# Optimization experiments

Hardware: AMD Instinct MI355X
Metric: run time of the kernel (lower is better)

## Reference

```python
import jax, jax.numpy as jnp
import numpy as np

N_NODES = 100000
N_EDGES = 3200000
D_IN = 64
D_HID = 64


def _sage_conv(x, src, dst, Wl, bl, Wr, n_nodes):
    # PyG SAGEConv (aggr='mean', root_weight=True):
    #   out = lin_l(mean_{j in N(i)} x_j) + lin_r(x_i)
    msg = x[src]                                              # [E, d] gather
    agg = jax.ops.segment_sum(msg, dst, num_segments=n_nodes) # [N, d] scatter-sum
    cnt = jax.ops.segment_sum(jnp.ones((src.shape[0],), x.dtype), dst,
                              num_segments=n_nodes)           # [N]
    agg = agg / jnp.maximum(cnt, 1.0)[:, None]                # mean (empty -> 0)
    return agg @ Wl.T + bl + x @ Wr.T


def setup_inputs() -> dict:
    key = jax.random.key(0)
    ks = jax.random.split(key, 12)
    x = jax.random.normal(ks[0], (N_NODES, D_IN), dtype=jnp.float32)
    edge_index = jax.random.randint(ks[1], (2, N_EDGES), 0, N_NODES, dtype=jnp.int64)
    s = 1.0 / np.sqrt(D_IN)
    h = 1.0 / np.sqrt(D_HID)
    params = {
        'Wl1': jax.random.uniform(ks[2], (D_HID, D_IN), jnp.float32, -s, s),
        'bl1': jnp.zeros((D_HID,), jnp.float32),
        'Wr1': jax.random.uniform(ks[3], (D_HID, D_IN), jnp.float32, -s, s),
        'Wl2': jax.random.uniform(ks[4], (D_HID, D_HID), jnp.float32, -h, h),
        'bl2': jnp.zeros((D_HID,), jnp.float32),
        'Wr2': jax.random.uniform(ks[5], (D_HID, D_HID), jnp.float32, -h, h),
        'Wl3': jax.random.uniform(ks[6], (D_HID, D_HID), jnp.float32, -h, h),
        'bl3': jnp.zeros((D_HID,), jnp.float32),
        'Wr3': jax.random.uniform(ks[7], (D_HID, D_HID), jnp.float32, -h, h),
        'Wlin': jax.random.uniform(ks[8], (1, D_HID), jnp.float32, -h, h),
        'blin': jnp.zeros((1,), jnp.float32),
    }
    return {'x': x, 'edge_index': edge_index, **params}


def reference(x, edge_index, Wl1, bl1, Wr1, Wl2, bl2, Wr2, Wl3, bl3, Wr3, Wlin, blin):
    src, dst = edge_index[0], edge_index[1]
    n = x.shape[0]
    h = _sage_conv(x, src, dst, Wl1, bl1, Wr1, n)
    h = _sage_conv(h, src, dst, Wl2, bl2, Wr2, n)
    h = _sage_conv(h, src, dst, Wl3, bl3, Wr3, n)
    # global_mean_pool with batch=None -> single graph mean over all nodes
    g = jnp.mean(h, axis=0, keepdims=True)   # [1, D_HID]
    return g @ Wlin.T + blin                 # [1, 1]
```

## Files before the change

kernel.cpp:

```cpp
#include <hip/hip_runtime.h>
#include <stdint.h>

#define D 64
#define PNBLK 512
#define NBMAX 400
#define CAPS 16
#define CAPD 32
#define XPB 512
#define XPST 272

__device__ __forceinline__ uint32_t rup8(uint32_t v) { return (v + 7u) & ~7u; }

__global__ void zero_kernel(float* __restrict__ p, int n) {
    int i = blockIdx.x * blockDim.x + threadIdx.x;
    if (i < n) p[i] = 0.0f;
}

__global__ void cnt_kernel(const int* __restrict__ dst, float* __restrict__ cnt, int ne) {
    int i = blockIdx.x * blockDim.x + threadIdx.x;
    if (i < ne) atomicAdd(&cnt[dst[i]], 1.0f);
}
__global__ void scatter_kernel(const int* __restrict__ src, const int* __restrict__ dst,
                               const float* __restrict__ r, float* __restrict__ an, int ne) {
    int i = blockIdx.x * blockDim.x + threadIdx.x;
    if (i < ne) atomicAdd(&an[src[i]], r[dst[i]]);
}
__global__ void r0_kernel(const float* __restrict__ cnt, float* __restrict__ r, int nn) {
    int i = blockIdx.x * blockDim.x + threadIdx.x;
    if (i < nn) r[i] = (1.0f / (float)nn) / fmaxf(cnt[i], 1.0f);
}
__global__ void rdiv_kernel(const float* __restrict__ a, const float* __restrict__ cnt,
                            float* __restrict__ r, int nn) {
    int i = blockIdx.x * blockDim.x + threadIdx.x;
    if (i < nn) r[i] = a[i] / fmaxf(cnt[i], 1.0f);
}

__global__ __launch_bounds__(256) void xpass_kernel(
        const float* __restrict__ x,
        const float* __restrict__ a1, const float* __restrict__ a2,
        const float* __restrict__ a3, float* __restrict__ Xpart, int nn) {
    const int tid = threadIdx.x;
    const int cg = tid & 15;
    const int rs = tid >> 4;
    float4 c0 = {0,0,0,0}, c1 = {0,0,0,0}, c2 = {0,0,0,0}, c3 = {0,0,0,0};
    float ss1 = 0.f, ss2 = 0.f;
    for (int i = blockIdx.x * 16 + rs; i < nn; i += gridDim.x * 16) {
        float4 xv = *(const float4*)(x + (size_t)i * D + cg * 4);
        float w1 = a1[i], w2 = a2[i], w3 = a3[i];
        c0.x += xv.x; c0.y += xv.y; c0.z += xv.z; c0.w += xv.w;
        c1.x = fmaf(w1, xv.x, c1.x); c1.y = fmaf(w1, xv.y, c1.y);
        c1.z = fmaf(w1, xv.z, c1.z); c1.w = fmaf(w1, xv.w, c1.w);
        c2.x = fmaf(w2, xv.x, c2.x); c2.y = fmaf(w2, xv.y, c2.y);
        c2.z = fmaf(w2, xv.z, c2.z); c2.w = fmaf(w2, xv.w, c2.w);
        c3.x = fmaf(w3, xv.x, c3.x); c3.y = fmaf(w3, xv.y, c3.y);
        c3.z = fmaf(w3, xv.z, c3.z); c3.w = fmaf(w3, xv.w, c3.w);
        if (cg == 0) { ss1 += w1; ss2 += w2; }
    }
    __shared__ float4 sm[4][16][16];
    __shared__ float sms1[16], sms2[16];
    sm[0][rs][cg] = c0; sm[1][rs][cg] = c1; sm[2][rs][cg] = c2; sm[3][rs][cg] = c3;
    if (cg == 0) { sms1[rs] = ss1; sms2[rs] = ss2; }
    __syncthreads();
    for (int s = 8; s; s >>= 1) {
        if (rs < s) {
            #pragma unroll
            for (int k = 0; k < 4; k++) {
                float4 a = sm[k][rs][cg], b = sm[k][rs + s][cg];
                a.x += b.x; a.y += b.y; a.z += b.z; a.w += b.w;
                sm[k][rs][cg] = a;
            }
            if (cg == 0) { sms1[rs] += sms1[rs + s]; sms2[rs] += sms2[rs + s]; }
        }
        __syncthreads();
    }
    float* outp = Xpart + (size_t)blockIdx.x * XPST;
    {
        int k = tid >> 6, col = tid & 63;
        outp[tid] = ((const float*)&sm[k][0][col >> 2])[col & 3];
    }
    if (tid == 0) outp[256] = sms1[0];
    if (tid == 1) outp[257] = sms2[0];
}


__global__ __launch_bounds__(512) void hist_kernel(
        const int* __restrict__ src, const int* __restrict__ dst,
        uint32_t* __restrict__ blkhistS, uint32_t* __restrict__ blkhistD,
        int ne, int nb, int chunk) {
    __shared__ uint32_t hS[4][NBMAX], hD[4][NBMAX];
    const int T = blockDim.x, tid = threadIdx.x;
    for (int i = tid; i < nb; i += T) {
        hS[0][i] = 0u; hS[1][i] = 0u; hS[2][i] = 0u; hS[3][i] = 0u;
        hD[0][i] = 0u; hD[1][i] = 0u; hD[2][i] = 0u; hD[3][i] = 0u;
    }
    __syncthreads();
    const int cp = tid & 3;
    int beg = blockIdx.x * chunk;
    int end = min(beg + chunk, ne);
    for (int base = beg; base < end; base += T * 4) {
        int e0 = base + tid * 4;
        if (e0 + 3 < end) {
            int4 s4 = *(const int4*)(src + e0);
            int4 d4 = *(const int4*)(dst + e0);
            atomicAdd(&hS[cp][((uint32_t)s4.x) >> 8], 1u);
            atomicAdd(&hS[cp][((uint32_t)s4.y) >> 8], 1u);
            atomicAdd(&hS[cp][((uint32_t)s4.z) >> 8], 1u);
            atomicAdd(&hS[cp][((uint32_t)s4.w) >> 8], 1u);
            atomicAdd(&hD[cp][((uint32_t)d4.x) >> 8], 1u);
            atomicAdd(&hD[cp][((uint32_t)d4.y) >> 8], 1u);
            atomicAdd(&hD[cp][((uint32_t)d4.z) >> 8], 1u);
            atomicAdd(&hD[cp][((uint32_t)d4.w) >> 8], 1u);
        } else {
            for (int k = 0; k < 4; k++) {
                int e = e0 + k;
                if (e < end) {
                    atomicAdd(&hS[cp][((uint32_t)src[e]) >> 8], 1u);
                    atomicAdd(&hD[cp][((uint32_t)dst[e]) >> 8], 1u);
                }
            }
        }
    }
    __syncthreads();
    for (int i = tid; i < nb; i += T) {
        blkhistS[(size_t)blockIdx.x * nb + i] = hS[0][i] + hS[1][i] + hS[2][i] + hS[3][i];
        blkhistD[(size_t)blockIdx.x * nb + i] = hD[0][i] + hD[1][i] + hD[2][i] + hD[3][i];
    }
}

__global__ __launch_bounds__(64) void reduceoffs_kernel(
        const uint32_t* __restrict__ blkhistS, const uint32_t* __restrict__ blkhistD,
        uint32_t* __restrict__ offsS, uint32_t* __restrict__ offsD,
        uint32_t* __restrict__ totS, uint32_t* __restrict__ totD, int nb) {
    int which = (blockIdx.x >= nb) ? 1 : 0;
    int b = blockIdx.x - which * nb;
    const uint32_t* bh = which ? blkhistD : blkhistS;
    uint32_t* of       = which ? offsD    : offsS;
    uint32_t* to       = which ? totD     : totS;
    int lane = threadIdx.x;
    const int K = PNBLK / 64;
    uint32_t v[K];
    uint32_t s = 0;
    int base = lane * K;
    #pragma unroll
    for (int k = 0; k < K; k++) {
        uint32_t c = bh[(size_t)(base + k) * nb + b];
        v[k] = which ? c : rup8(c);
        s += v[k];
    }
    uint32_t inc = s;
    #pragma unroll
    for (int off = 1; off < 64; off <<= 1) {
        uint32_t nbr = __shfl_up(inc, off, 64);
        if (lane >= off) inc += nbr;
    }
    uint32_t run = inc - s;
    #pragma unroll
    for (int k = 0; k < K; k++) { of[(size_t)(base + k) * nb + b] = run; run += v[k]; }
    if (lane == 63) to[b] = inc;
}

__global__ __launch_bounds__(512) void scan_kernel(
        const uint32_t* __restrict__ totS, const uint32_t* __restrict__ totD,
        uint32_t* __restrict__ bstartS, uint32_t* __restrict__ bstartD, int nb) {
    const int isS = (blockIdx.x == 0);
    const uint32_t* to = isS ? totS : totD;
    uint32_t* bs       = isS ? bstartS : bstartD;
    const int tid = threadIdx.x;
    uint32_t tot = (tid < nb) ? to[tid] : 0u;
    int lane = tid & 63, wid = tid >> 6;
    uint32_t incl = tot;
    #pragma unroll
    for (int off = 1; off < 64; off <<= 1) {
        uint32_t nbr = __shfl_up(incl, off, 64);
        if (lane >= off) incl += nbr;
    }
    __shared__ uint32_t wsum[8];
    if (lane == 63) wsum[wid] = incl;
    __syncthreads();
    if (wid == 0 && lane < 8) {
        uint32_t w = wsum[lane], wi = w;
        #pragma unroll
        for (int off = 1; off < 8; off <<= 1) {
            uint32_t nbr = __shfl_up(wi, off, 8);
            if (lane >= off) wi += nbr;
        }
        wsum[lane] = wi - w;
    }
    __syncthreads();
    uint32_t excl = incl - tot + wsum[wid];
    if (tid < nb) bs[tid] = excl;
    if (tid == nb - 1) bs[nb] = excl + tot;
}

__global__ __launch_bounds__(512) void place_kernel(
        const int* __restrict__ src, const int* __restrict__ dst,
        const uint32_t* __restrict__ offsS, const uint32_t* __restrict__ offsD,
        const uint32_t* __restrict__ bstartS, const uint32_t* __restrict__ bstartD,
        uint32_t* __restrict__ sortedS, uint8_t* __restrict__ sortedD,
        int ne, int nb, int chunk, uint32_t sentinel) {
    __shared__ uint32_t stS[NBMAX * CAPS];
    __shared__ uint8_t  stD[NBMAX * CAPD];
    __shared__ uint32_t pendS[NBMAX], pendD[NBMAX];
    __shared__ uint32_t gposS[NBMAX], gposD[NBMAX];
    __shared__ int again;
    const int T = blockDim.x, tid = threadIdx.x;
    for (int i = tid; i < nb; i += T) {
        pendS[i] = 0u; pendD[i] = 0u;
        gposS[i] = bstartS[i] + offsS[(size_t)blockIdx.x * nb + i];
        gposD[i] = bstartD[i] + offsD[(size_t)blockIdx.x * nb + i];
    }
    __syncthreads();
    int beg = blockIdx.x * chunk;
    int end = min(beg + chunk, ne);
    for (int base = beg; base < end; base += T * 4) {
        uint32_t vS[4]; uint8_t vD[4]; int bS[4], bD[4]; bool hS[4], hD[4];
        int e0 = base + tid * 4;
        if (e0 + 3 < end) {
            int4 s4 = *(const int4*)(src + e0);
            int4 d4 = *(const int4*)(dst + e0);
            int sv[4] = {s4.x, s4.y, s4.z, s4.w};
            int dv[4] = {d4.x, d4.y, d4.z, d4.w};
            #pragma unroll
            for (int k = 0; k < 4; k++) {
                uint32_t s = (uint32_t)sv[k], d = (uint32_t)dv[k];
                bS[k] = s >> 8; vS[k] = ((s & 255u) << 17) | d;
                bD[k] = d >> 8; vD[k] = (uint8_t)(d & 255u);
                hS[k] = true; hD[k] = true;
            }
        } else {
            #pragma unroll
            for (int k = 0; k < 4; k++) {
                int e = e0 + k;
                bool ok = e < end;
                hS[k] = ok; hD[k] = ok;
                if (ok) {
                    uint32_t s = (uint32_t)src[e], d = (uint32_t)dst[e];
                    bS[k] = s >> 8; vS[k] = ((s & 255u) << 17) | d;
                    bD[k] = d >> 8; vD[k] = (uint8_t)(d & 255u);
                } else { bS[k] = 0; bD[k] = 0; vS[k] = 0; vD[k] = 0; }
            }
        }
        while (true) {
            if (tid == 0) again = 0;
            __syncthreads();
            #pragma unroll
            for (int k = 0; k < 4; k++) {
                if (hS[k]) {
                    uint32_t p = atomicAdd(&pendS[bS[k]], 1u);
                    if (p < CAPS) { stS[bS[k] * CAPS + p] = vS[k]; hS[k] = false; }
                }
                if (hD[k]) {
                    uint32_t p = atomicAdd(&pendD[bD[k]], 1u);
                    if (p < CAPD) { stD[bD[k] * CAPD + p] = vD[k]; hD[k] = false; }
                }
            }
            if (hS[0] | hS[1] | hS[2] | hS[3] | hD[0] | hD[1] | hD[2] | hD[3]) again = 1;
            __syncthreads();
            for (int bb = tid; bb < nb; bb += T) {
                uint32_t n = min(pendS[bb], (uint32_t)CAPS);
                if (n == CAPS) {
                    uint32_t g = gposS[bb];
                    uint4* dstp = (uint4*)(sortedS + g);
                    const uint4* srcp = (const uint4*)(stS + bb * CAPS);
                    dstp[0] = srcp[0]; dstp[1] = srcp[1];
                    dstp[2] = srcp[2]; dstp[3] = srcp[3];
                    gposS[bb] = g + CAPS;
                    pendS[bb] = 0u;
                } else pendS[bb] = n;
                n = min(pendD[bb], (uint32_t)CAPD);
                if (n == CAPD) {
                    uint32_t g = gposD[bb];
                    #pragma unroll
                    for (int k = 0; k < CAPD; k++) sortedD[g + k] = stD[bb * CAPD + k];
                    gposD[bb] = g + CAPD;
                    pendD[bb] = 0u;
                } else pendD[bb] = n;
            }
            __syncthreads();
            const int cont = again;
            __syncthreads();
            if (!cont) break;
        }
    }
    for (int bb = tid; bb < nb; bb += T) {
        uint32_t n = pendS[bb];
        if (n > 0) {
            uint32_t g = gposS[bb];
            uint32_t m = rup8(n);
            uint32_t tmp[CAPS];
            for (uint32_t k = 0; k < m; k++) tmp[k] = (k < n) ? stS[bb * CAPS + k] : sentinel;
            for (uint32_t k = 0; k < m; k += 8) {
                uint4* dstp = (uint4*)(sortedS + g + k);
                dstp[0] = *(const uint4*)(tmp + k);
                dstp[1] = *(const uint4*)(tmp + k + 4);
            }
        }
        uint32_t nD = pendD[bb], gD = gposD[bb];
        for (uint32_t k = 0; k < nD; k++) sortedD[gD + k] = stD[bb * CAPD + k];
    }
}

__global__ __launch_bounds__(512) void cntb_kernel(
        const uint8_t* __restrict__ sortedD, const uint32_t* __restrict__ bstartD,
        float* __restrict__ cnt, float* __restrict__ rA, float* __restrict__ rB,
        int nn, float invN) {
    int b = blockIdx.x, tid = threadIdx.x;
    __shared__ uint32_t c[2][256];
    ((uint32_t*)c)[tid] = 0u;
    __syncthreads();
    const int cp = tid & 1;
    uint32_t beg = bstartD[b], end = bstartD[b + 1];
    for (uint32_t e = beg + tid; e < end; e += 512) atomicAdd(&c[cp][sortedD[e]], 1u);
    __syncthreads();
    if (b == 0 && tid == 0) { rA[nn] = 0.0f; rB[nn] = 0.0f; }
    int v = b * 256 + tid;
    if (tid < 256 && v < nn) {
        float cf = (float)(c[0][tid] + c[1][tid]);
        cnt[v] = cf;
        rA[v] = invN / fmaxf(cf, 1.0f);
    }
}

__global__ __launch_bounds__(512) void scatb_kernel(
        const uint32_t* __restrict__ sortedS, const uint32_t* __restrict__ bstartS,
        const float* __restrict__ rin, const float* __restrict__ cnt,
        float* __restrict__ aout, float* __restrict__ rout, int nn) {
    int b = blockIdx.x, tid = threadIdx.x;
    __shared__ float acc[2][256];
    ((float*)acc)[tid] = 0.0f;
    __syncthreads();
    const int cp = tid & 1;
    uint32_t beg = bstartS[b], end = bstartS[b + 1];
    for (uint32_t e = beg + tid * 4; e < end; e += 512 * 4) {
        uint4 p = *(const uint4*)(sortedS + e);
        atomicAdd(&acc[cp][p.x >> 17], rin[p.x & 0x1FFFFu]);
        atomicAdd(&acc[cp][p.y >> 17], rin[p.y & 0x1FFFFu]);
        atomicAdd(&acc[cp][p.z >> 17], rin[p.z & 0x1FFFFu]);
        atomicAdd(&acc[cp][p.w >> 17], rin[p.w & 0x1FFFFu]);
    }
    __syncthreads();
    int v = b * 256 + tid;
    if (tid < 256 && v < nn) {
        float a = acc[0][tid] + acc[1][tid];
        aout[v] = a;
        if (rout) rout[v] = a / fmaxf(cnt[v], 1.0f);
    }
}

__global__ __launch_bounds__(512) void scatx_kernel(
        const uint32_t* __restrict__ sortedS, const uint32_t* __restrict__ bstartS,
        const float* __restrict__ rin, const float* __restrict__ x,
        const float* __restrict__ a1, const float* __restrict__ a2,
        float* __restrict__ Xpart, int nn) {
    const int b = blockIdx.x, tid = threadIdx.x;
    __shared__ float acc[2][256];
    ((float*)acc)[tid] = 0.0f;
    __syncthreads();
    const int cp = tid & 1;
    uint32_t beg = bstartS[b], end = bstartS[b + 1];
    for (uint32_t e = beg + tid * 4; e < end; e += 512 * 4) {
        uint4 p = *(const uint4*)(sortedS + e);
        atomicAdd(&acc[cp][p.x >> 17], rin[p.x & 0x1FFFFu]);
        atomicAdd(&acc[cp][p.y >> 17], rin[p.y & 0x1FFFFu]);
        atomicAdd(&acc[cp][p.z >> 17], rin[p.z & 0x1FFFFu]);
        atomicAdd(&acc[cp][p.w >> 17], rin[p.w & 0x1FFFFu]);
    }
    __syncthreads();
    const int cg = tid & 15, rs = tid >> 4;
    float4 c0 = {0,0,0,0}, c1 = {0,0,0,0}, c2 = {0,0,0,0}, c3 = {0,0,0,0};
    float ss1 = 0.f, ss2 = 0.f;
    const int vbase = b * 256;
    for (int r = rs; r < 256; r += 32) {
        int v = vbase + r;
        if (v >= nn) break;
        float4 xv = *(const float4*)(x + (size_t)v * D + cg * 4);
        float w1 = a1[v], w2 = a2[v];
        float w3 = acc[0][r] + acc[1][r];
        c0.x += xv.x; c0.y += xv.y; c0.z += xv.z; c0.w += xv.w;
        c1.x = fmaf(w1, xv.x, c1.x); c1.y = fmaf(w1, xv.y, c1.y);
        c1.z = fmaf(w1, xv.z, c1.z); c1.w = fmaf(w1, xv.w, c1.w);
        c2.x = fmaf(w2, xv.x, c2.x); c2.y = fmaf(w2, xv.y, c2.y);
        c2.z = fmaf(w2, xv.z, c2.z); c2.w = fmaf(w2, xv.w, c2.w);
        c3.x = fmaf(w3, xv.x, c3.x); c3.y = fmaf(w3, xv.y, c3.y);
        c3.z = fmaf(w3, xv.z, c3.z); c3.w = fmaf(w3, xv.w, c3.w);
        if (cg == 0) { ss1 += w1; ss2 += w2; }
    }
    __shared__ float4 sm[4][32][16];
    __shared__ float sms1[32], sms2[32];
    sm[0][rs][cg] = c0; sm[1][rs][cg] = c1; sm[2][rs][cg] = c2; sm[3][rs][cg] = c3;
    if (cg == 0) { sms1[rs] = ss1; sms2[rs] = ss2; }
    __syncthreads();
    for (int s = 16; s; s >>= 1) {
        if (rs < s) {
            #pragma unroll
            for (int k = 0; k < 4; k++) {
                float4 a = sm[k][rs][cg], bb = sm[k][rs + s][cg];
                a.x += bb.x; a.y += bb.y; a.z += bb.z; a.w += bb.w;
                sm[k][rs][cg] = a;
            }
            if (cg == 0) { sms1[rs] += sms1[rs + s]; sms2[rs] += sms2[rs + s]; }
        }
        __syncthreads();
    }
    float* outp = Xpart + (size_t)b * XPST;
    if (tid < 256) {
        int k = tid >> 6, col = tid & 63;
        outp[tid] = ((const float*)&sm[k][0][col >> 2])[col & 3];
    }
    if (tid == 0) outp[256] = sms1[0];
    if (tid == 1) outp[257] = sms2[0];
}

__global__ __launch_bounds__(64) void xreduce_kernel(
        const float* __restrict__ Xpart, float* __restrict__ X, int nxb) {
    int j = blockIdx.x;
    int lane = threadIdx.x;
    float s = 0.f;
    for (int b = lane; b < nxb; b += 64) s += Xpart[(size_t)b * XPST + j];
    #pragma unroll
    for (int off = 32; off; off >>= 1) s += __shfl_down(s, off);
    if (lane == 0) X[j] = s;
}

__global__ __launch_bounds__(256) void final_kernel(const float* __restrict__ X,
    const float* __restrict__ Wl1, const float* __restrict__ bl1, const float* __restrict__ Wr1,
    const float* __restrict__ Wl2, const float* __restrict__ bl2, const float* __restrict__ Wr2,
    const float* __restrict__ Wl3, const float* __restrict__ bl3, const float* __restrict__ Wr3,
    const float* __restrict__ Wlin, const float* __restrict__ blin,
    float* __restrict__ out, int nn) {
    const int tid = threadIdx.x;
    const int t = tid >> 2, q = tid & 3, c0 = q * 16;
    __shared__ float X1[D], X2[D], X3[D], X4[D];
    __shared__ float m1u[D], m1a1[D], m1a2[D], m2u[D], m2a1[D];
    __shared__ float sred[4];
    if (tid < 64)       X1[tid]       = X[tid] * (1.0f / (float)nn);
    else if (tid < 128) X2[tid - 64]  = X[tid];
    else if (tid < 192) X3[tid - 128] = X[tid];
    else                X4[tid - 192] = X[tid];
    const float s1 = X[4 * D], s2 = X[4 * D + 1];
    __syncthreads();

    float dl2 = 0.f, dl3 = 0.f, dl4 = 0.f, dr1 = 0.f, dr2 = 0.f, dr3 = 0.f;
    #pragma unroll
    for (int k = 0; k < 16; k++) {
        int c = c0 + k;
        float wl = Wl1[t * D + c], wr = Wr1[t * D + c];
        dl2 = fmaf(wl, X2[c], dl2); dl3 = fmaf(wl, X3[c], dl3); dl4 = fmaf(wl, X4[c], dl4);
        dr1 = fmaf(wr, X1[c], dr1); dr2 = fmaf(wr, X2[c], dr2); dr3 = fmaf(wr, X3[c], dr3);
    }
    #define RED4(v) { v += __shfl_down(v, 2, 4); v += __shfl_down(v, 1, 4); }
    RED4(dl2) RED4(dl3) RED4(dl4) RED4(dr1) RED4(dr2) RED4(dr3)
    if (q == 0) {
        m1u[t]  = dl2 + bl1[t]      + dr1;
        m1a1[t] = dl3 + bl1[t] * s1 + dr2;
        m1a2[t] = dl4 + bl1[t] * s2 + dr3;
    }
    __syncthreads();

    float el1 = 0.f, el2 = 0.f, er0 = 0.f, er1 = 0.f;
    #pragma unroll
    for (int k = 0; k < 16; k++) {
        int c = c0 + k;
        float wl = Wl2[t * D + c], wr = Wr2[t * D + c];
        el1 = fmaf(wl, m1a1[c], el1); el2 = fmaf(wl, m1a2[c], el2);
        er0 = fmaf(wr, m1u[c],  er0); er1 = fmaf(wr, m1a1[c], er1);
    }
    RED4(el1) RED4(el2) RED4(er0) RED4(er1)
    if (q == 0) {
        m2u[t]  = el1 + bl2[t]      + er0;
        m2a1[t] = el2 + bl2[t] * s1 + er1;
    }
    __syncthreads();

    float fl = 0.f, fr = 0.f;
    #pragma unroll
    for (int k = 0; k < 16; k++) {
        int c = c0 + k;
        fl = fmaf(Wl3[t * D + c], m2a1[c], fl);
        fr = fmaf(Wr3[t * D + c], m2u[c],  fr);
    }
    RED4(fl) RED4(fr)
    float contrib = 0.f;
    if (q == 0) contrib = Wlin[t] * (fl + bl3[t] + fr);
    #pragma unroll
    for (int off = 32; off; off >>= 1) contrib += __shfl_down(contrib, off);
    if ((tid & 63) == 0) sred[tid >> 6] = contrib;
    __syncthreads();
    if (tid == 0) out[0] = sred[0] + sred[1] + sred[2] + sred[3] + blin[0];
}

extern "C" void kernel_launch(void* const* d_in, const int* in_sizes, int n_in,
                              void* d_out, int out_size, void* d_ws, size_t ws_size,
                              hipStream_t stream) {
    const float* x    = (const float*)d_in[0];
    const int*   ei   = (const int*)d_in[1];
    const float* Wl1  = (const float*)d_in[2];
    const float* bl1  = (const float*)d_in[3];
    const float* Wr1  = (const float*)d_in[4];
    const float* Wl2  = (const float*)d_in[5];
    const float* bl2  = (const float*)d_in[6];
    const float* Wr2  = (const float*)d_in[7];
    const float* Wl3  = (const float*)d_in[8];
    const float* bl3  = (const float*)d_in[9];
    const float* Wr3  = (const float*)d_in[10];
    const float* Wlin = (const float*)d_in[11];
    const float* blin = (const float*)d_in[12];
    float* out = (float*)d_out;

    const int nn = in_sizes[0] / D;
    const int ne = in_sizes[1] / 2;
    const int* srcIdx = ei;
    const int* dstIdx = ei + ne;
    const int nb = (nn + 255) >> 8;

    char* base = (char*)d_ws;
    size_t cur = 0;
    auto alloc = [&](size_t bytes) -> void* {
        void* p = base + cur;
        cur = (cur + bytes + 255) & ~(size_t)255;
        return p;
    };
    float*    cnt      = (float*)alloc((size_t)nn * 4);
    float*    a1       = (float*)alloc((size_t)nn * 4);
    float*    a2       = (float*)alloc((size_t)nn * 4);
    float*    a3       = (float*)alloc((size_t)nn * 4);
    float*    rA       = (float*)alloc((size_t)(nn + 1) * 4);
    float*    rB       = (float*)alloc((size_t)(nn + 1) * 4);
    float*    X        = (float*)alloc((4 * D + 2) * 4);
    float*    Xpart    = (float*)alloc((size_t)XPB * XPST * 4);
    size_t    zend     = cur;
    uint32_t* blkhistS = (uint32_t*)alloc((size_t)PNBLK * nb * 4);
    uint32_t* blkhistD = (uint32_t*)alloc((size_t)PNBLK * nb * 4);
    uint32_t* offsS    = (uint32_t*)alloc((size_t)PNBLK * nb * 4);
    uint32_t* offsD    = (uint32_t*)alloc((size_t)PNBLK * nb * 4);
    uint32_t* bstartS  = (uint32_t*)alloc((size_t)(nb + 1) * 4);
    uint32_t* bstartD  = (uint32_t*)alloc((size_t)(nb + 1) * 4);
    uint32_t* totS     = (uint32_t*)alloc((size_t)nb * 4);
    uint32_t* totD     = (uint32_t*)alloc((size_t)nb * 4);
    uint32_t* sortedS  = (uint32_t*)alloc(((size_t)ne + (size_t)PNBLK * nb * 7) * 4);
    uint8_t*  sortedD  = (uint8_t*)alloc((size_t)ne);
    const size_t need = cur;

    const int B = 256;
    if (need <= ws_size && nn <= 131071 && nb <= NBMAX) {
        const int chunk = ((ne + PNBLK - 1) / PNBLK + 3) & ~3;
        hipLaunchKernelGGL(hist_kernel, dim3(PNBLK), dim3(512), 0, stream,
                           srcIdx, dstIdx, blkhistS, blkhistD, ne, nb, chunk);
        hipLaunchKernelGGL(reduceoffs_kernel, dim3(2 * nb), dim3(64), 0, stream,
                           blkhistS, blkhistD, offsS, offsD, totS, totD, nb);
        hipLaunchKernelGGL(scan_kernel, dim3(2), dim3(512), 0, stream,
                           totS, totD, bstartS, bstartD, nb);
        hipLaunchKernelGGL(place_kernel, dim3(PNBLK), dim3(512), 0, stream,
                           srcIdx, dstIdx, offsS, offsD, bstartS, bstartD,
                           sortedS, sortedD, ne, nb, chunk, (uint32_t)nn);
        hipLaunchKernelGGL(cntb_kernel, dim3(nb), dim3(512), 0, stream,
                           sortedD, bstartD, cnt, rA, rB, nn, 1.0f / (float)nn);
        hipLaunchKernelGGL(scatb_kernel, dim3(nb), dim3(512), 0, stream,
                           sortedS, bstartS, rA, cnt, a1, rB, nn);
        hipLaunchKernelGGL(scatb_kernel, dim3(nb), dim3(512), 0, stream,
                           sortedS, bstartS, rB, cnt, a2, rA, nn);
        hipLaunchKernelGGL(scatx_kernel, dim3(nb), dim3(512), 0, stream,
                           sortedS, bstartS, rA, x, a1, a2, Xpart, nn);
        hipLaunchKernelGGL(xreduce_kernel, dim3(4 * D + 2), dim3(64), 0, stream,
                           Xpart, X, nb);
    } else {
        const int zn = (int)(zend / 4);
        hipLaunchKernelGGL(zero_kernel, dim3((zn + B - 1) / B), dim3(B), 0, stream, (float*)d_ws, zn);
        hipLaunchKernelGGL(cnt_kernel,  dim3((ne + B - 1) / B), dim3(B), 0, stream, dstIdx, cnt, ne);
        hipLaunchKernelGGL(r0_kernel,   dim3((nn + B - 1) / B), dim3(B), 0, stream, cnt, rA, nn);
        hipLaunchKernelGGL(scatter_kernel, dim3((ne + B - 1) / B), dim3(B), 0, stream, srcIdx, dstIdx, rA, a1, ne);
        hipLaunchKernelGGL(rdiv_kernel, dim3((nn + B - 1) / B), dim3(B), 0, stream, a1, cnt, rA, nn);
        hipLaunchKernelGGL(scatter_kernel, dim3((ne + B - 1) / B), dim3(B), 0, stream, srcIdx, dstIdx, rA, a2, ne);
        hipLaunchKernelGGL(rdiv_kernel, dim3((nn + B - 1) / B), dim3(B), 0, stream, a2, cnt, rA, nn);
        hipLaunchKernelGGL(scatter_kernel, dim3((ne + B - 1) / B), dim3(B), 0, stream, srcIdx, dstIdx, rA, a3, ne);
        hipLaunchKernelGGL(xpass_kernel, dim3(XPB), dim3(B), 0, stream, x, a1, a2, a3, Xpart, nn);
        hipLaunchKernelGGL(xreduce_kernel, dim3(4 * D + 2), dim3(64), 0, stream, Xpart, X, XPB);
    }

    hipLaunchKernelGGL(final_kernel, dim3(1), dim3(B), 0, stream, X,
                       Wl1, bl1, Wr1, Wl2, bl2, Wr2, Wl3, bl3, Wr3, Wlin, blin, out, nn);
}
```

Baseline: 153.3 us.

## Split scatter passes across two blocks per bucket with float2 partials, unfuse x-pass

Each bucket's scatter pass now runs as two blocks, each covering half of the sorted edge range. The blocks write separate halves of a float2 partial result pre-scaled by 1/count, and the consumer sums the halves, so the launch gets twice as many blocks. The LDS accumulator is privatized four ways instead of two, and the edge loop processes eight edges per iteration to expose more gathers in flight. The third scatter no longer fuses the x-weighted reduction; a separate grid-stride xpass2 kernel rereads x and recombines the partials. The aim is better CU occupancy and less LDS atomic contention, at the cost of an extra kernel and doubled partial-array traffic.

Result: slower. 158.3 us (+3.3%).

```diff
diff --git a/kernel.cpp b/kernel.cpp
--- a/kernel.cpp
+++ b/kernel.cpp
@@ -302,80 +302,87 @@
 
 __global__ __launch_bounds__(512) void cntb_kernel(
         const uint8_t* __restrict__ sortedD, const uint32_t* __restrict__ bstartD,
-        float* __restrict__ cnt, float* __restrict__ rA, float* __restrict__ rB,
+        float* __restrict__ cnt, float* __restrict__ invcnt,
+        float2* __restrict__ rp0, float2* __restrict__ rp1,
+        float2* __restrict__ rp2, float2* __restrict__ rp3,
         int nn, float invN) {
     int b = blockIdx.x, tid = threadIdx.x;
-    __shared__ uint32_t c[2][256];
-    ((uint32_t*)c)[tid] = 0u;
-    __syncthreads();
-    const int cp = tid & 1;
+    __shared__ uint32_t c[4][256];
+    ((uint32_t*)c)[tid] = 0u; ((uint32_t*)c)[512 + tid] = 0u;
+    __syncthreads();
+    const int cp = tid & 3;
     uint32_t beg = bstartD[b], end = bstartD[b + 1];
     for (uint32_t e = beg + tid; e < end; e += 512) atomicAdd(&c[cp][sortedD[e]], 1u);
     __syncthreads();
-    if (b == 0 && tid == 0) { rA[nn] = 0.0f; rB[nn] = 0.0f; }
+    if (b == 0 && tid == 0) {
+        float2 z = make_float2(0.f, 0.f);
+        rp0[nn] = z; rp1[nn] = z; rp2[nn] = z; rp3[nn] = z;
+    }
     int v = b * 256 + tid;
     if (tid < 256 && v < nn) {
-        float cf = (float)(c[0][tid] + c[1][tid]);
+        float cf = (float)(c[0][tid] + c[1][tid] + c[2][tid] + c[3][tid]);
+        float ic = 1.0f / fmaxf(cf, 1.0f);
         cnt[v] = cf;
-        rA[v] = invN / fmaxf(cf, 1.0f);
-    }
-}
-
-__global__ __launch_bounds__(512) void scatb_kernel(
+        invcnt[v] = ic;
+        rp0[v] = make_float2(invN * ic, 0.f);
+    }
+}
+
+__global__ __launch_bounds__(512) void scats_kernel(
         const uint32_t* __restrict__ sortedS, const uint32_t* __restrict__ bstartS,
-        const float* __restrict__ rin, const float* __restrict__ cnt,
-        float* __restrict__ aout, float* __restrict__ rout, int nn) {
-    int b = blockIdx.x, tid = threadIdx.x;
-    __shared__ float acc[2][256];
-    ((float*)acc)[tid] = 0.0f;
-    __syncthreads();
-    const int cp = tid & 1;
+        const float2* __restrict__ rin, const float* __restrict__ invcnt,
+        float2* __restrict__ rout, int nn) {
+    const int b = blockIdx.x >> 1, h = blockIdx.x & 1;
+    const int tid = threadIdx.x;
+    __shared__ float acc[4][256];
+    ((float*)acc)[tid] = 0.0f; ((float*)acc)[512 + tid] = 0.0f;
+    __syncthreads();
+    const int cp = tid & 3;
     uint32_t beg = bstartS[b], end = bstartS[b + 1];
-    for (uint32_t e = beg + tid * 4; e < end; e += 512 * 4) {
-        uint4 p = *(const uint4*)(sortedS + e);
-        atomicAdd(&acc[cp][p.x >> 17], rin[p.x & 0x1FFFFu]);
-        atomicAdd(&acc[cp][p.y >> 17], rin[p.y & 0x1FFFFu]);
-        atomicAdd(&acc[cp][p.z >> 17], rin[p.z & 0x1FFFFu]);
-        atomicAdd(&acc[cp][p.w >> 17], rin[p.w & 0x1FFFFu]);
+    uint32_t nOct = (end - beg) >> 3;
+    uint32_t h0len = ((nOct + 1u) >> 1) << 3;
+    uint32_t myBeg = beg + (h ? h0len : 0u);
+    uint32_t myEnd = h ? end : (beg + h0len);
+    for (uint32_t e = myBeg + tid * 8; e < myEnd; e += 512 * 8) {
+        uint4 p0 = *(const uint4*)(sortedS + e);
+        uint4 p1 = *(const uint4*)(sortedS + e + 4);
+        float2 q0 = rin[p0.x & 0x1FFFFu], q1 = rin[p0.y & 0x1FFFFu];
+        float2 q2 = rin[p0.z & 0x1FFFFu], q3 = rin[p0.w & 0x1FFFFu];
+        float2 q4 = rin[p1.x & 0x1FFFFu], q5 = rin[p1.y & 0x1FFFFu];
+        float2 q6 = rin[p1.z & 0x1FFFFu], q7 = rin[p1.w & 0x1FFFFu];
+        atomicAdd(&acc[cp][p0.x >> 17], q0.x + q0.y);
+        atomicAdd(&acc[cp][p0.y >> 17], q1.x + q1.y);
+        atomicAdd(&acc[cp][p0.z >> 17], q2.x + q2.y);
+        atomicAdd(&acc[cp][p0.w >> 17], q3.x + q3.y);
+        atomicAdd(&acc[cp][p1.x >> 17], q4.x + q4.y);
+        atomicAdd(&acc[cp][p1.y >> 17], q5.x + q5.y);
+        atomicAdd(&acc[cp][p1.z >> 17], q6.x + q6.y);
+        atomicAdd(&acc[cp][p1.w >> 17], q7.x + q7.y);
     }
     __syncthreads();
     int v = b * 256 + tid;
     if (tid < 256 && v < nn) {
-        float a = acc[0][tid] + acc[1][tid];
-        aout[v] = a;
-        if (rout) rout[v] = a / fmaxf(cnt[v], 1.0f);
-    }
-}
-
-__global__ __launch_bounds__(512) void scatx_kernel(
-        const uint32_t* __restrict__ sortedS, const uint32_t* __restrict__ bstartS,
-        const float* __restrict__ rin, const float* __restrict__ x,
-        const float* __restrict__ a1, const float* __restrict__ a2,
-        float* __restrict__ Xpart, int nn) {
-    const int b = blockIdx.x, tid = threadIdx.x;
-    __shared__ float acc[2][256];
-    ((float*)acc)[tid] = 0.0f;
-    __syncthreads();
-    const int cp = tid & 1;
-    uint32_t beg = bstartS[b], end = bstartS[b + 1];
-    for (uint32_t e = beg + tid * 4; e < end; e += 512 * 4) {
-        uint4 p = *(const uint4*)(sortedS + e);
-        atomicAdd(&acc[cp][p.x >> 17], rin[p.x & 0x1FFFFu]);
-        atomicAdd(&acc[cp][p.y >> 17], rin[p.y & 0x1FFFFu]);
-        atomicAdd(&acc[cp][p.z >> 17], rin[p.z & 0x1FFFFu]);
-        atomicAdd(&acc[cp][p.w >> 17], rin[p.w & 0x1FFFFu]);
-    }
-    __syncthreads();
-    const int cg = tid & 15, rs = tid >> 4;
+        float part = acc[0][tid] + acc[1][tid] + acc[2][tid] + acc[3][tid];
+        ((float*)&rout[v])[h] = part * invcnt[v];
+    }
+}
+
+__global__ __launch_bounds__(256) void xpass2_kernel(
+        const float* __restrict__ x, const float* __restrict__ cnt,
+        const float2* __restrict__ rp1, const float2* __restrict__ rp2,
+        const float2* __restrict__ rp3, float* __restrict__ Xpart, int nn) {
+    const int tid = threadIdx.x;
+    const int cg = tid & 15;
+    const int rs = tid >> 4;
     float4 c0 = {0,0,0,0}, c1 = {0,0,0,0}, c2 = {0,0,0,0}, c3 = {0,0,0,0};
     float ss1 = 0.f, ss2 = 0.f;
-    const int vbase = b * 256;
-    for (int r = rs; r < 256; r += 32) {
-        int v = vbase + r;
-        if (v >= nn) break;
-        float4 xv = *(const float4*)(x + (size_t)v * D + cg * 4);
-        float w1 = a1[v], w2 = a2[v];
-        float w3 = acc[0][r] + acc[1][r];
+    for (int i = blockIdx.x * 16 + rs; i < nn; i += gridDim.x * 16) {
+        float4 xv = *(const float4*)(x + (size_t)i * D + cg * 4);
+        float cf = cnt[i];
+        float2 q1 = rp1[i], q2 = rp2[i], q3 = rp3[i];
+        float w1 = (q1.x + q1.y) * cf;
+        float w2 = (q2.x + q2.y) * cf;
+        float w3 = (q3.x + q3.y) * cf;
         c0.x += xv.x; c0.y += xv.y; c0.z += xv.z; c0.w += xv.w;
         c1.x = fmaf(w1, xv.x, c1.x); c1.y = fmaf(w1, xv.y, c1.y);
         c1.z = fmaf(w1, xv.z, c1.z); c1.w = fmaf(w1, xv.w, c1.w);
@@ -385,25 +392,25 @@
         c3.z = fmaf(w3, xv.z, c3.z); c3.w = fmaf(w3, xv.w, c3.w);
         if (cg == 0) { ss1 += w1; ss2 += w2; }
     }
-    __shared__ float4 sm[4][32][16];
-    __shared__ float sms1[32], sms2[32];
+    __shared__ float4 sm[4][16][16];
+    __shared__ float sms1[16], sms2[16];
     sm[0][rs][cg] = c0; sm[1][rs][cg] = c1; sm[2][rs][cg] = c2; sm[3][rs][cg] = c3;
     if (cg == 0) { sms1[rs] = ss1; sms2[rs] = ss2; }
     __syncthreads();
-    for (int s = 16; s; s >>= 1) {
+    for (int s = 8; s; s >>= 1) {
         if (rs < s) {
             #pragma unroll
             for (int k = 0; k < 4; k++) {
-                float4 a = sm[k][rs][cg], bb = sm[k][rs + s][cg];
-                a.x += bb.x; a.y += bb.y; a.z += bb.z; a.w += bb.w;
+                float4 a = sm[k][rs][cg], b = sm[k][rs + s][cg];
+                a.x += b.x; a.y += b.y; a.z += b.z; a.w += b.w;
                 sm[k][rs][cg] = a;
             }
             if (cg == 0) { sms1[rs] += sms1[rs + s]; sms2[rs] += sms2[rs + s]; }
         }
         __syncthreads();
     }
-    float* outp = Xpart + (size_t)b * XPST;
-    if (tid < 256) {
+    float* outp = Xpart + (size_t)blockIdx.x * XPST;
+    {
         int k = tid >> 6, col = tid & 63;
         outp[tid] = ((const float*)&sm[k][0][col >> 2])[col & 3];
     }
@@ -525,10 +532,13 @@
     float*    a2       = (float*)alloc((size_t)nn * 4);
     float*    a3       = (float*)alloc((size_t)nn * 4);
     float*    rA       = (float*)alloc((size_t)(nn + 1) * 4);
-    float*    rB       = (float*)alloc((size_t)(nn + 1) * 4);
+    float*    invcnt   = (float*)alloc((size_t)nn * 4);
+    float2*   rp0      = (float2*)alloc((size_t)(nn + 1) * 8);
+    float2*   rp1      = (float2*)alloc((size_t)(nn + 1) * 8);
+    float2*   rp2      = (float2*)alloc((size_t)(nn + 1) * 8);
+    float2*   rp3      = (float2*)alloc((size_t)(nn + 1) * 8);
     float*    X        = (float*)alloc((4 * D + 2) * 4);
     float*    Xpart    = (float*)alloc((size_t)XPB * XPST * 4);
-    size_t    zend     = cur;
     uint32_t* blkhistS = (uint32_t*)alloc((size_t)PNBLK * nb * 4);
     uint32_t* blkhistD = (uint32_t*)alloc((size_t)PNBLK * nb * 4);
     uint32_t* offsS    = (uint32_t*)alloc((size_t)PNBLK * nb * 4);
@@ -554,17 +564,20 @@
                            srcIdx, dstIdx, offsS, offsD, bstartS, bstartD,
                            sortedS, sortedD, ne, nb, chunk, (uint32_t)nn);
         hipLaunchKernelGGL(cntb_kernel, dim3(nb), dim3(512), 0, stream,
-                           sortedD, bstartD, cnt, rA, rB, nn, 1.0f / (float)nn);
-        hipLaunchKernelGGL(scatb_kernel, dim3(nb), dim3(512), 0, stream,
-                           sortedS, bstartS, rA, cnt, a1, rB, nn);
-        hipLaunchKernelGGL(scatb_kernel, dim3(nb), dim3(512), 0, stream,
-                           sortedS, bstartS, rB, cnt, a2, rA, nn);
-        hipLaunchKernelGGL(scatx_kernel, dim3(nb), dim3(512), 0, stream,
-                           sortedS, bstartS, rA, x, a1, a2, Xpart, nn);
+                           sortedD, bstartD, cnt, invcnt, rp0, rp1, rp2, rp3,
+                           nn, 1.0f / (float)nn);
+        hipLaunchKernelGGL(scats_kernel, dim3(2 * nb), dim3(512), 0, stream,
+                           sortedS, bstartS, rp0, invcnt, rp1, nn);
+        hipLaunchKernelGGL(scats_kernel, dim3(2 * nb), dim3(512), 0, stream,
+                           sortedS, bstartS, rp1, invcnt, rp2, nn);
+        hipLaunchKernelGGL(scats_kernel, dim3(2 * nb), dim3(512), 0, stream,
+                           sortedS, bstartS, rp2, invcnt, rp3, nn);
+        hipLaunchKernelGGL(xpass2_kernel, dim3(XPB), dim3(B), 0, stream,
+                           x, cnt, rp1, rp2, rp3, Xpart, nn);
         hipLaunchKernelGGL(xreduce_kernel, dim3(4 * D + 2), dim3(64), 0, stream,
-                           Xpart, X, nb);
+                           Xpart, X, XPB);
     } else {
-        const int zn = (int)(zend / 4);
+        const int zn = 4 * nn + (nn + 1);
         hipLaunchKernelGGL(zero_kernel, dim3((zn + B - 1) / B), dim3(B), 0, stream, (float*)d_ws, zn);
         hipLaunchKernelGGL(cnt_kernel,  dim3((ne + B - 1) / B), dim3(B), 0, stream, dstIdx, cnt, ne);
         hipLaunchKernelGGL(r0_kernel,   dim3((nn + B - 1) / B), dim3(B), 0, stream, cnt, rA, nn);
```
